# Optimization experiments

Hardware: AMD Instinct MI355X
Metric: run time of the kernel (lower is better)

## Reference

```python
import jax, jax.numpy as jnp
import numpy as np

B, L, H = 16, 4096, 512
NT = 8                      # num_time_enc_dims
IN = 2 + NT                 # input_proj in-features
OUT = 2 * H + NT            # bi-directional output size
HH = max(32, H // 2)        # gauss head hidden
EPS = 1e-5


def setup_inputs() -> dict:
    key = jax.random.key(0)
    ks = jax.random.split(key, 24)
    w = lambda k, *s: (jax.random.normal(k, s, dtype=jnp.float32) * 0.05)
    return {
        "x": jax.random.normal(ks[0], (B, L, 2), dtype=jnp.float32),
        "t": jax.random.uniform(ks[1], (B, L), dtype=jnp.float32),
        # time encoder: Linear(1,8) -> ReLU -> Linear(8,8)
        "te_w1": w(ks[2], NT, 1), "te_b1": w(ks[3], NT),
        "te_w2": w(ks[4], NT, NT), "te_b2": w(ks[5], NT),
        # input projections (IN -> H)
        "fproj_w": w(ks[6], H, IN), "fproj_b": w(ks[7], H),
        "bproj_w": w(ks[8], H, IN), "bproj_b": w(ks[9], H),
        # minGRU cells (H -> H)
        "fz_w": w(ks[10], H, H), "fz_b": w(ks[11], H),
        "fh_w": w(ks[12], H, H), "fh_b": w(ks[13], H),
        "bz_w": w(ks[14], H, H), "bz_b": w(ks[15], H),
        "bh_w": w(ks[16], H, H), "bh_b": w(ks[17], H),
        # head norm + time scale
        "ln_g": jnp.ones((OUT,), jnp.float32), "ln_b": jnp.zeros((OUT,), jnp.float32),
        "time_scale": jnp.float32(5.0),
        # gauss head: Linear(OUT,HH) -> GELU -> Linear(HH,1)
        "gh_w1": w(ks[18], HH, OUT), "gh_b1": w(ks[19], HH),
        "gh_w2": w(ks[20], 1, HH), "gh_b2": w(ks[21], 1),
    }


def _mingru_parallel(xp, wz, bz, wh, bh):
    # xp: (B, L, H) projected inputs; h0 = 0
    z = jax.nn.sigmoid(xp @ wz.T + bz)          # (B,L,H)
    h_tilde = xp @ wh.T + bh                    # NOTE: no tanh in parallel mode
    a = 1.0 - z
    b = z * h_tilde
    A = jnp.cumprod(a, axis=1)
    B_div = b / jnp.clip(A, 1e-12)              # h0 = 0 so only the cumsum term
    return A * jnp.cumsum(B_div, axis=1)        # (B,L,H)


def reference(x, t, te_w1, te_b1, te_w2, te_b2,
              fproj_w, fproj_b, bproj_w, bproj_b,
              fz_w, fz_b, fh_w, fh_b, bz_w, bz_b, bh_w, bh_b,
              ln_g, ln_b, time_scale, gh_w1, gh_b1, gh_w2, gh_b2):
    # time encoding
    ts = (t - t[:, :1])[..., None]                              # (B,L,1)
    te = jax.nn.relu(ts @ te_w1.T + te_b1) @ te_w2.T + te_b2    # (B,L,NT)
    xc = jnp.concatenate([x, te], axis=-1)                      # (B,L,IN)

    # backward direction: scan over reversed sequence, then shift left
    xb = xc[:, ::-1]
    hb = _mingru_parallel(xb @ bproj_w.T + bproj_b, bz_w, bz_b, bh_w, bh_b)[:, ::-1]
    hb = jnp.concatenate([hb[:, 1:], jnp.zeros_like(hb[:, :1])], axis=1)

    # forward direction: scan, then shift right
    hf = _mingru_parallel(xc @ fproj_w.T + fproj_b, fz_w, fz_b, fh_w, fh_b)
    hf = jnp.concatenate([jnp.zeros_like(hf[:, :1]), hf[:, :-1]], axis=1)

    h_bi = jnp.concatenate([hf, hb, te], axis=-1)               # (B,L,OUT)
    mu = h_bi.mean(axis=-1, keepdims=True)
    var = ((h_bi - mu) ** 2).mean(axis=-1, keepdims=True)
    hn = (h_bi - mu) / jnp.sqrt(var + EPS) * ln_g + ln_b
    hn = jnp.concatenate([hn[..., :-NT], hn[..., -NT:] * time_scale], axis=-1)

    h1 = jax.nn.gelu(hn @ gh_w1.T + gh_b1, approximate=False)
    return h1 @ gh_w2.T + gh_b2                                 # (B,L,1)
```

## Files before the change

kernel.cpp:

```cpp
#include <hip/hip_runtime.h>
#include <hip/hip_bf16.h>

constexpr int cB  = 16;
constexpr int cL  = 4096;
constexpr int cH  = 512;
constexpr int cN  = cB * cL;
constexpr int cOUT = 1032;
constexpr int cHH = 256;
constexpr float cEPS = 1e-5f;

constexpr int cSL  = 256;

constexpr size_t OFF_XC    = 0;
constexpr size_t SZ_XC     = (size_t)10 * cN;
constexpr size_t OFF_WZ    = OFF_XC + SZ_XC;
constexpr size_t OFF_WH    = OFF_WZ + 2 * 512 * 12;
constexpr size_t OFF_BZ    = OFF_WH + 2 * 512 * 12;
constexpr size_t OFF_BH    = OFF_BZ + 2 * 512;
constexpr size_t OFF_W1GT  = OFF_BH + 2 * 512;
constexpr size_t OFF_SW    = OFF_W1GT + (size_t)cOUT * cHH;
constexpr size_t OFF_CB    = OFF_SW + cHH;
constexpr size_t OFF_HT    = OFF_CB + cHH;

__device__ __forceinline__ float gelu_f(float h1) {
    float xx = h1 * 0.70710678118654752f;
    float ax = fabsf(xx);
    float t = __fdividef(1.f, 1.f + 0.3275911f * ax);
    float poly = t * (0.254829592f + t * (-0.284496736f +
                 t * (1.421413741f + t * (-1.453152027f + t * 1.061405429f))));
    float er = 1.f - poly * __expf(-ax * ax);
    er = copysignf(er, xx);
    return 0.5f * h1 * (1.f + er);
}

__global__ void __launch_bounds__(256) k_prep_all(
    const float* __restrict__ x, const float* __restrict__ tarr,
    const float* __restrict__ tw1, const float* __restrict__ tb1,
    const float* __restrict__ tw2, const float* __restrict__ tb2,
    const float* __restrict__ fproj_w, const float* __restrict__ fproj_b,
    const float* __restrict__ bproj_w, const float* __restrict__ bproj_b,
    const float* __restrict__ fz_w, const float* __restrict__ fz_b,
    const float* __restrict__ fh_w, const float* __restrict__ fh_b,
    const float* __restrict__ bz_w, const float* __restrict__ bz_b,
    const float* __restrict__ bh_w, const float* __restrict__ bh_b,
    const float* __restrict__ ln_g, const float* __restrict__ ln_b,
    const float* __restrict__ tsc, const float* __restrict__ gh_w1,
    const float* __restrict__ gh_b1, const float* __restrict__ b2p,
    float* __restrict__ Wz, float* __restrict__ Wh,
    float* __restrict__ bz, float* __restrict__ bh,
    float* __restrict__ W1gT, float* __restrict__ SW, float* __restrict__ cb,
    float* __restrict__ xcS, float* __restrict__ out)
{
    __shared__ float smem[32 * 257];
    int bx = blockIdx.x;
    int tid = threadIdx.x;

    if (bx < 512) {
        float* spw = smem;
        float* spb = smem + 5120;
        int m = bx >> 7;
        int hblk = bx & 127;
        int dir = m >> 1;
        const float* gw = (m == 0) ? fz_w : (m == 1) ? fh_w : (m == 2) ? bz_w : bh_w;
        const float* gb = (m == 0) ? fz_b : (m == 1) ? fh_b : (m == 2) ? bz_b : bh_b;
        const float* pw = dir ? bproj_w : fproj_w;
        const float* pb = dir ? bproj_b : fproj_b;
        for (int i = tid; i < 5120; i += 256) spw[i] = pw[i];
        spb[tid] = pb[tid]; spb[tid + 256] = pb[tid + 256];
        __syncthreads();

        int wv = tid >> 6, lane = tid & 63;
        int h = hblk * 4 + wv;
        float acc[11];
#pragma unroll
        for (int k = 0; k < 11; ++k) acc[k] = 0.f;
#pragma unroll
        for (int it = 0; it < 8; ++it) {
            int j = it * 64 + lane;
            float g = gw[(size_t)h * 512 + j];
#pragma unroll
            for (int k = 0; k < 10; ++k) acc[k] += g * spw[j * 10 + k];
            acc[10] += g * spb[j];
        }
#pragma unroll
        for (int k = 0; k < 11; ++k) {
#pragma unroll
            for (int off = 32; off; off >>= 1) acc[k] += __shfl_down(acc[k], off, 64);
        }
        if (lane == 0) {
            float* Wout = (m & 1) ? Wh : Wz;
            float* bout = (m & 1) ? bh : bz;
            float* wrow = Wout + ((size_t)dir * 512 + h) * 12;
#pragma unroll
            for (int k = 0; k < 10; ++k) wrow[k] = acc[k];
            wrow[10] = 0.f; wrow[11] = 0.f;
            bout[dir * 512 + h] = acc[10] + gb[h];
        }
    } else if (bx < 545) {
        int k0 = (bx - 512) * 32;
        for (int idx = tid; idx < 32 * 256; idx += 256) {
            int j = idx >> 5, kk = idx & 31;
            int k = k0 + kk;
            smem[kk * 257 + j] = (k < cOUT) ? gh_w1[(size_t)j * cOUT + k] : 0.f;
        }
        __syncthreads();
        float ts = tsc[0];
        for (int idx = tid; idx < 32 * 256; idx += 256) {
            int kk = idx >> 8, j = idx & 255;
            int k = k0 + kk;
            if (k < cOUT) {
                float sc = ln_g[k] * (k >= 2 * cH ? ts : 1.f);
                W1gT[(size_t)k * cHH + j] = smem[kk * 257 + j] * sc;
            }
        }
    } else if (bx < 801) {
        int j = bx - 545;
        float ts = tsc[0];
        float ag = 0.f, ab = 0.f;
        for (int k = tid; k < cOUT; k += 256) {
            float w = gh_w1[(size_t)j * cOUT + k];
            float sc = (k >= 2 * cH) ? ts : 1.f;
            ag += w * ln_g[k] * sc;
            ab += w * ln_b[k] * sc;
        }
#pragma unroll
        for (int off = 32; off; off >>= 1) {
            ag += __shfl_down(ag, off, 64);
            ab += __shfl_down(ab, off, 64);
        }
        int wv = tid >> 6, lane = tid & 63;
        if (lane == 0) { smem[wv] = ag; smem[4 + wv] = ab; }
        __syncthreads();
        if (tid == 0) {
            SW[j] = smem[0] + smem[1] + smem[2] + smem[3];
            cb[j] = gh_b1[j] + smem[4] + smem[5] + smem[6] + smem[7];
        }
    } else {
        int idx = (bx - 801) * 256 + tid;
        int b = idx >> 12;
        float ts = tarr[idx] - tarr[b << 12];
        float hid[8];
#pragma unroll
        for (int i = 0; i < 8; ++i) {
            float v = ts * tw1[i] + tb1[i];
            hid[i] = v > 0.f ? v : 0.f;
        }
        xcS[idx]      = x[idx * 2];
        xcS[cN + idx] = x[idx * 2 + 1];
#pragma unroll
        for (int o = 0; o < 8; ++o) {
            float v = tb2[o];
#pragma unroll
            for (int i = 0; i < 8; ++i) v += tw2[o * 8 + i] * hid[i];
            xcS[(size_t)(2 + o) * cN + idx] = v;
        }
        int t = idx & (cL - 1);
        bool bnd = (t >= 1 && t <= cSL) || (t >= cL - 1 - cSL && t <= cL - 2);
        if (bnd) out[idx] = b2p[0];
    }
}

__global__ void __launch_bounds__(256) k_scan3(
    const float* __restrict__ xcS, const float* __restrict__ Wz,
    const float* __restrict__ Wh, const float* __restrict__ bzv,
    const float* __restrict__ bhv, float* __restrict__ hT)
{
    __shared__ float sxc[10 * 256];
    __shared__ float chA[4][64];
    __shared__ float chS[4][64];
    __shared__ float T[4][32 * 64];
    int tid = threadIdx.x;
    int w = tid >> 6, lane = tid & 63;
    int bx = blockIdx.x;
    int hg = bx & 7, b = (bx >> 3) & 15, dir = bx >> 7;
    int h = hg * 64 + lane;

    const float* wzp = Wz + ((size_t)dir * 512 + h) * 12;
    const float* whp = Wh + ((size_t)dir * 512 + h) * 12;
    float wz[10], wh[10];
#pragma unroll
    for (int k = 0; k < 10; ++k) { wz[k] = wzp[k]; wh[k] = whp[k]; }
    float bz = bzv[dir * 512 + h];
    float bh = bhv[dir * 512 + h];

    size_t base = (size_t)b * cL;
    for (int idx = tid; idx < 2560; idx += 256) {
        int c = idx >> 8, s = idx & 255;
        int tI = dir ? (cL - 1 - s) : s;
        sxc[idx] = xcS[(size_t)c * cN + base + tI];
    }
    __syncthreads();

    int p0 = w * 64;
    {
        float Aloc = 1.f;
#pragma unroll 2
        for (int i = 0; i < 64; ++i) {
            int p = p0 + i;
            float lz = bz;
#pragma unroll
            for (int c = 0; c < 10; ++c) lz += wz[c] * sxc[c * 256 + p];
            float z = 1.f / (1.f + __expf(-lz));
            Aloc *= (1.f - z);
        }
        chA[w][lane] = Aloc;
    }
    __syncthreads();
    float Apre = 1.f;
    for (int cc = 0; cc < w; ++cc) Apre *= chA[cc][lane];

    {
        float A = Apre, Sl = 0.f;
#pragma unroll 2
        for (int i = 0; i < 64; ++i) {
            int p = p0 + i;
            float lz = bz, lh = bh;
#pragma unroll
            for (int c = 0; c < 10; ++c) {
                float xv = sxc[c * 256 + p];
                lz += wz[c] * xv;
                lh += wh[c] * xv;
            }
            float z = 1.f / (1.f + __expf(-lz));
            A *= (1.f - z);
            Sl += __fdividef(z * lh, fmaxf(A, 1e-12f));
        }
        chS[w][lane] = Sl;
    }
    __syncthreads();
    float Spre = 0.f;
    for (int cc = 0; cc < w; ++cc) Spre += chS[cc][lane];

    size_t htrow = ((size_t)(dir * 16 + b) * 512 + hg * 64) * cSL;
    float A2 = Apre, S2 = Spre;
    float* Tw = T[w];
#pragma unroll
    for (int sub = 0; sub < 2; ++sub) {
#pragma unroll 2
        for (int i = 0; i < 32; ++i) {
            int p = p0 + sub * 32 + i;
            float lz = bz, lh = bh;
#pragma unroll
            for (int c = 0; c < 10; ++c) {
                float xv = sxc[c * 256 + p];
                lz += wz[c] * xv;
                lh += wh[c] * xv;
            }
            float z = 1.f / (1.f + __expf(-lz));
            A2 *= (1.f - z);
            S2 += __fdividef(z * lh, fmaxf(A2, 1e-12f));
            Tw[i * 64 + ((lane + i) & 63)] = A2 * S2;
        }
        int q = lane & 31;
        int choff = lane >> 5;
        int pq = p0 + sub * 32 + q;
        int qglob = dir ? (cSL - 1 - pq) : pq;
#pragma unroll 8
        for (int it = 0; it < 32; ++it) {
            int ch = it * 2 + choff;
            float val = Tw[q * 64 + ((ch + q) & 63)];
            hT[htrow + (size_t)ch * cSL + qglob] = val;
        }
    }
}

__global__ void __launch_bounds__(256) k_out_all(
    const float* __restrict__ xcS, const float* __restrict__ hT,
    const float* __restrict__ W1gT, const float* __restrict__ SW,
    const float* __restrict__ cb, const float* __restrict__ w2,
    const float* __restrict__ b2p, float* __restrict__ out)
{
    int bx = blockIdx.x;
    int tid = threadIdx.x;
    if (bx < 512) {
        int lane = tid & 63;
        int wq = __builtin_amdgcn_readfirstlane(tid >> 6);
        int jq = bx & 3;
        int rgid = bx >> 2;
        int dir = rgid >> 6;
        int rem = rgid & 63;
        int b   = rem >> 2;
        int rg  = rem & 3;
        int jbase = jq * 64 + wq * 16;
        int rw = rg * 64 + lane;
        size_t grow = (size_t)b * cL + (dir ? 3839 : 1) + rw;

        const float* Xp = hT + ((size_t)(dir * 16 + b) * 512) * cSL + rw;
        const float* Wp = W1gT + ((size_t)(dir * 512)) * cHH + jbase;

        float acc[16];
#pragma unroll
        for (int jj = 0; jj < 16; ++jj) acc[jj] = 0.f;
        float s1 = 0.f, s2 = 0.f;
#pragma unroll 4
        for (int k = 0; k < 512; ++k) {
            float xv = Xp[(size_t)k * cSL];
            const float* wr = Wp + (size_t)k * cHH;
            s1 += xv; s2 += xv * xv;
#pragma unroll
            for (int jj = 0; jj < 16; ++jj) acc[jj] += wr[jj] * xv;
        }

        float te[8];
        float tsum = 0.f, tsq = 0.f;
#pragma unroll
        for (int i = 0; i < 8; ++i) {
            float v = xcS[(size_t)(2 + i) * cN + grow];
            te[i] = v; tsum += v; tsq += v * v;
        }
        float mu = (s1 + tsum) * (1.f / cOUT);
        float rs = rsqrtf((s2 + tsq) * (1.f / cOUT) - mu * mu + cEPS);

        float tot = 0.f;
#pragma unroll
        for (int jj = 0; jj < 16; ++jj) {
            int j = jbase + jj;
            float a = acc[jj];
#pragma unroll
            for (int i = 0; i < 8; ++i)
                a += W1gT[(size_t)(2 * cH + i) * cHH + j] * te[i];
            float h1 = (a - mu * SW[j]) * rs + cb[j];
            tot += gelu_f(h1) * w2[j];
        }
        atomicAdd(&out[grow], tot);
    } else {
        int bx2 = bx - 512;
        int sub = tid >> 6;
        int lane = tid & 63;
        int row = bx2 * 4 + sub;
        int t = row & (cL - 1);
        bool bnd = (t >= 1 && t <= cSL) || (t >= cL - 1 - cSL && t <= cL - 2);
        if (bnd) return;
        float te[8];
#pragma unroll
        for (int i = 0; i < 8; ++i) te[i] = xcS[(size_t)(2 + i) * cN + row];
        float s1 = 0.f, s2 = 0.f;
#pragma unroll
        for (int i = 0; i < 8; ++i) { s1 += te[i]; s2 += te[i] * te[i]; }
        float mu = s1 * (1.f / cOUT);
        float rs = rsqrtf(s2 * (1.f / cOUT) - mu * mu + cEPS);
        float tot = 0.f;
#pragma unroll
        for (int jj = 0; jj < 4; ++jj) {
            int j = lane + jj * 64;
            float a = 0.f;
#pragma unroll
            for (int i = 0; i < 8; ++i)
                a += W1gT[(size_t)(2 * cH + i) * cHH + j] * te[i];
            float h1 = (a - mu * SW[j]) * rs + cb[j];
            tot += gelu_f(h1) * w2[j];
        }
#pragma unroll
        for (int off = 32; off; off >>= 1) tot += __shfl_down(tot, off, 64);
        if (lane == 0) out[row] = tot + b2p[0];
    }
}

extern "C" void kernel_launch(void* const* d_in, const int* in_sizes, int n_in,
                              void* d_out, int out_size, void* d_ws, size_t ws_size,
                              hipStream_t stream)
{
    (void)in_sizes; (void)n_in; (void)out_size; (void)ws_size;
    const float* x       = (const float*)d_in[0];
    const float* tarr    = (const float*)d_in[1];
    const float* te_w1   = (const float*)d_in[2];
    const float* te_b1   = (const float*)d_in[3];
    const float* te_w2   = (const float*)d_in[4];
    const float* te_b2   = (const float*)d_in[5];
    const float* fproj_w = (const float*)d_in[6];
    const float* fproj_b = (const float*)d_in[7];
    const float* bproj_w = (const float*)d_in[8];
    const float* bproj_b = (const float*)d_in[9];
    const float* fz_w    = (const float*)d_in[10];
    const float* fz_b    = (const float*)d_in[11];
    const float* fh_w    = (const float*)d_in[12];
    const float* fh_b    = (const float*)d_in[13];
    const float* bz_w    = (const float*)d_in[14];
    const float* bz_b    = (const float*)d_in[15];
    const float* bh_w    = (const float*)d_in[16];
    const float* bh_b    = (const float*)d_in[17];
    const float* ln_g    = (const float*)d_in[18];
    const float* ln_b    = (const float*)d_in[19];
    const float* tsc     = (const float*)d_in[20];
    const float* gh_w1   = (const float*)d_in[21];
    const float* gh_b1   = (const float*)d_in[22];
    const float* gh_w2   = (const float*)d_in[23];
    const float* gh_b2   = (const float*)d_in[24];

    float* ws = (float*)d_ws;
    float* xcS   = ws + OFF_XC;
    float* Wz    = ws + OFF_WZ;
    float* Wh    = ws + OFF_WH;
    float* bzv   = ws + OFF_BZ;
    float* bhv   = ws + OFF_BH;
    float* W1gT  = ws + OFF_W1GT;
    float* SWv   = ws + OFF_SW;
    float* cbv   = ws + OFF_CB;
    float* hT    = ws + OFF_HT;
    float* out   = (float*)d_out;

    k_prep_all<<<1057, 256, 0, stream>>>(
        x, tarr, te_w1, te_b1, te_w2, te_b2,
        fproj_w, fproj_b, bproj_w, bproj_b,
        fz_w, fz_b, fh_w, fh_b, bz_w, bz_b, bh_w, bh_b,
        ln_g, ln_b, tsc, gh_w1, gh_b1, gh_b2,
        Wz, Wh, bzv, bhv, W1gT, SWv, cbv, xcS, out);
    k_scan3<<<256, 256, 0, stream>>>(xcS, Wz, Wh, bzv, bhv, hT);
    k_out_all<<<512 + (cB * cL) / 4, 256, 0, stream>>>(
        xcS, hT, W1gT, SWv, cbv, gh_w2, gh_b2, out);
}
```

Baseline: 206.0 us.

## Pack scan inputs row-major, use packed FP32 math, batch interior rows per wave

The scan kernel's shared-memory input tile moves from channel-major to a per-position 12-float layout, so each position's gate inputs load as three float4 reads. The output kernel's boundary GEMV and gate math use 2-wide vector float types, which should let the compiler emit packed FP32 FMAs. The interior-row path is reorganised so each wave keeps its time-encoding weights in registers and processes 16 rows in a loop, cutting the grid from tens of thousands of blocks to 1536. The trade-off is less parallelism per row, plus possible LDS bank conflicts from the new layout.

```diff
diff --git a/kernel.cpp b/kernel.cpp
--- a/kernel.cpp
+++ b/kernel.cpp
@@ -1,5 +1,7 @@
 #include <hip/hip_runtime.h>
 #include <hip/hip_bf16.h>
+
+typedef float v2f __attribute__((ext_vector_type(2)));
 
 constexpr int cB  = 16;
 constexpr int cL  = 4096;
@@ -165,7 +167,7 @@
     const float* __restrict__ Wh, const float* __restrict__ bzv,
     const float* __restrict__ bhv, float* __restrict__ hT)
 {
-    __shared__ float sxc[10 * 256];
+    __shared__ __align__(16) float sxc[256 * 12];
     __shared__ float chA[4][64];
     __shared__ float chS[4][64];
     __shared__ float T[4][32 * 64];
@@ -187,19 +189,41 @@
     for (int idx = tid; idx < 2560; idx += 256) {
         int c = idx >> 8, s = idx & 255;
         int tI = dir ? (cL - 1 - s) : s;
-        sxc[idx] = xcS[(size_t)c * cN + base + tI];
+        sxc[s * 12 + c] = xcS[(size_t)c * cN + base + tI];
+    }
+    for (int idx = tid; idx < 512; idx += 256) {
+        int s = idx & 255;
+        sxc[s * 12 + 10 + (idx >> 8)] = 0.f;
     }
     __syncthreads();
+
+#define GATE_LZ(p, lzv)                                                       \
+    {                                                                         \
+        const float4* xp_ = (const float4*)(sxc + (p) * 12);                  \
+        float4 a0_ = xp_[0], a1_ = xp_[1], a2_ = xp_[2];                      \
+        lzv = bz + wz[0]*a0_.x + wz[1]*a0_.y + wz[2]*a0_.z + wz[3]*a0_.w      \
+                 + wz[4]*a1_.x + wz[5]*a1_.y + wz[6]*a1_.z + wz[7]*a1_.w      \
+                 + wz[8]*a2_.x + wz[9]*a2_.y;                                 \
+    }
+#define GATE_BOTH(p, lzv, lhv)                                                \
+    {                                                                         \
+        const float4* xp_ = (const float4*)(sxc + (p) * 12);                  \
+        float4 a0_ = xp_[0], a1_ = xp_[1], a2_ = xp_[2];                      \
+        lzv = bz + wz[0]*a0_.x + wz[1]*a0_.y + wz[2]*a0_.z + wz[3]*a0_.w      \
+                 + wz[4]*a1_.x + wz[5]*a1_.y + wz[6]*a1_.z + wz[7]*a1_.w      \
+                 + wz[8]*a2_.x + wz[9]*a2_.y;                                 \
+        lhv = bh + wh[0]*a0_.x + wh[1]*a0_.y + wh[2]*a0_.z + wh[3]*a0_.w      \
+                 + wh[4]*a1_.x + wh[5]*a1_.y + wh[6]*a1_.z + wh[7]*a1_.w      \
+                 + wh[8]*a2_.x + wh[9]*a2_.y;                                 \
+    }
 
     int p0 = w * 64;
     {
         float Aloc = 1.f;
 #pragma unroll 2
         for (int i = 0; i < 64; ++i) {
-            int p = p0 + i;
-            float lz = bz;
-#pragma unroll
-            for (int c = 0; c < 10; ++c) lz += wz[c] * sxc[c * 256 + p];
+            float lz;
+            GATE_LZ(p0 + i, lz);
             float z = 1.f / (1.f + __expf(-lz));
             Aloc *= (1.f - z);
         }
@@ -213,14 +237,8 @@
         float A = Apre, Sl = 0.f;
 #pragma unroll 2
         for (int i = 0; i < 64; ++i) {
-            int p = p0 + i;
-            float lz = bz, lh = bh;
-#pragma unroll
-            for (int c = 0; c < 10; ++c) {
-                float xv = sxc[c * 256 + p];
-                lz += wz[c] * xv;
-                lh += wh[c] * xv;
-            }
+            float lz, lh;
+            GATE_BOTH(p0 + i, lz, lh);
             float z = 1.f / (1.f + __expf(-lz));
             A *= (1.f - z);
             Sl += __fdividef(z * lh, fmaxf(A, 1e-12f));
@@ -239,13 +257,8 @@
 #pragma unroll 2
         for (int i = 0; i < 32; ++i) {
             int p = p0 + sub * 32 + i;
-            float lz = bz, lh = bh;
-#pragma unroll
-            for (int c = 0; c < 10; ++c) {
-                float xv = sxc[c * 256 + p];
-                lz += wz[c] * xv;
-                lh += wh[c] * xv;
-            }
+            float lz, lh;
+            GATE_BOTH(p, lz, lh);
             float z = 1.f / (1.f + __expf(-lz));
             A2 *= (1.f - z);
             S2 += __fdividef(z * lh, fmaxf(A2, 1e-12f));
@@ -262,6 +275,8 @@
             hT[htrow + (size_t)ch * cSL + qglob] = val;
         }
     }
+#undef GATE_LZ
+#undef GATE_BOTH
 }
 
 __global__ void __launch_bounds__(256) k_out_all(
@@ -286,19 +301,20 @@
         size_t grow = (size_t)b * cL + (dir ? 3839 : 1) + rw;
 
         const float* Xp = hT + ((size_t)(dir * 16 + b) * 512) * cSL + rw;
-        const float* Wp = W1gT + ((size_t)(dir * 512)) * cHH + jbase;
-
-        float acc[16];
-#pragma unroll
-        for (int jj = 0; jj < 16; ++jj) acc[jj] = 0.f;
+        const float* Wpb = W1gT + ((size_t)(dir * 512)) * cHH + jbase;
+
+        v2f acc2[8];
+#pragma unroll
+        for (int jj = 0; jj < 8; ++jj) acc2[jj] = (v2f){0.f, 0.f};
         float s1 = 0.f, s2 = 0.f;
 #pragma unroll 4
         for (int k = 0; k < 512; ++k) {
             float xv = Xp[(size_t)k * cSL];
-            const float* wr = Wp + (size_t)k * cHH;
+            const v2f* wr2 = (const v2f*)(Wpb + (size_t)k * cHH);
+            v2f xv2 = (v2f){xv, xv};
             s1 += xv; s2 += xv * xv;
 #pragma unroll
-            for (int jj = 0; jj < 16; ++jj) acc[jj] += wr[jj] * xv;
+            for (int jj = 0; jj < 8; ++jj) acc2[jj] += wr2[jj] * xv2;
         }
 
         float te[8];
@@ -310,49 +326,73 @@
         }
         float mu = (s1 + tsum) * (1.f / cOUT);
         float rs = rsqrtf((s2 + tsq) * (1.f / cOUT) - mu * mu + cEPS);
+        v2f mu2 = (v2f){mu, mu}, rs2 = (v2f){rs, rs};
 
         float tot = 0.f;
 #pragma unroll
-        for (int jj = 0; jj < 16; ++jj) {
-            int j = jbase + jj;
-            float a = acc[jj];
-#pragma unroll
-            for (int i = 0; i < 8; ++i)
-                a += W1gT[(size_t)(2 * cH + i) * cHH + j] * te[i];
-            float h1 = (a - mu * SW[j]) * rs + cb[j];
-            tot += gelu_f(h1) * w2[j];
+        for (int jj = 0; jj < 8; ++jj) {
+            v2f a2 = acc2[jj];
+#pragma unroll
+            for (int i = 0; i < 8; ++i) {
+                v2f wte2 = *(const v2f*)(W1gT + (size_t)(2 * cH + i) * cHH + jbase + 2 * jj);
+                a2 += wte2 * (v2f){te[i], te[i]};
+            }
+            v2f sw2 = *(const v2f*)(SW + jbase + 2 * jj);
+            v2f cb2 = *(const v2f*)(cb + jbase + 2 * jj);
+            v2f w22 = *(const v2f*)(w2 + jbase + 2 * jj);
+            v2f h12 = (a2 - mu2 * sw2) * rs2 + cb2;
+            tot += gelu_f(h12.x) * w22.x + gelu_f(h12.y) * w22.y;
         }
         atomicAdd(&out[grow], tot);
     } else {
-        int bx2 = bx - 512;
+        int m = bx - 512;
         int sub = tid >> 6;
         int lane = tid & 63;
-        int row = bx2 * 4 + sub;
-        int t = row & (cL - 1);
-        bool bnd = (t >= 1 && t <= cSL) || (t >= cL - 1 - cSL && t <= cL - 2);
-        if (bnd) return;
-        float te[8];
-#pragma unroll
-        for (int i = 0; i < 8; ++i) te[i] = xcS[(size_t)(2 + i) * cN + row];
-        float s1 = 0.f, s2 = 0.f;
-#pragma unroll
-        for (int i = 0; i < 8; ++i) { s1 += te[i]; s2 += te[i] * te[i]; }
-        float mu = s1 * (1.f / cOUT);
-        float rs = rsqrtf(s2 * (1.f / cOUT) - mu * mu + cEPS);
-        float tot = 0.f;
-#pragma unroll
-        for (int jj = 0; jj < 4; ++jj) {
-            int j = lane + jj * 64;
-            float a = 0.f;
-#pragma unroll
-            for (int i = 0; i < 8; ++i)
-                a += W1gT[(size_t)(2 * cH + i) * cHH + j] * te[i];
-            float h1 = (a - mu * SW[j]) * rs + cb[j];
-            tot += gelu_f(h1) * w2[j];
-        }
-#pragma unroll
-        for (int off = 32; off; off >>= 1) tot += __shfl_down(tot, off, 64);
-        if (lane == 0) out[row] = tot + b2p[0];
+        int g = m * 4 + sub;
+        int j0 = lane * 4;
+
+        v2f wteA[8], wteB[8];
+#pragma unroll
+        for (int i = 0; i < 8; ++i) {
+            const float* wb = W1gT + (size_t)(2 * cH + i) * cHH + j0;
+            wteA[i] = *(const v2f*)wb;
+            wteB[i] = *(const v2f*)(wb + 2);
+        }
+        v2f swA = *(const v2f*)(SW + j0), swB = *(const v2f*)(SW + j0 + 2);
+        v2f cbA = *(const v2f*)(cb + j0), cbB = *(const v2f*)(cb + j0 + 2);
+        v2f w2A = *(const v2f*)(w2 + j0), w2B = *(const v2f*)(w2 + j0 + 2);
+        float b2 = b2p[0];
+
+        for (int r = 0; r < 16; ++r) {
+            int row = g * 16 + r;
+            int t = row & (cL - 1);
+            bool bnd = (t >= 1 && t <= cSL) || (t >= cL - 1 - cSL && t <= cL - 2);
+            if (bnd) continue;
+            float te[8];
+            float s1 = 0.f, s2 = 0.f;
+#pragma unroll
+            for (int i = 0; i < 8; ++i) {
+                float v = xcS[(size_t)(2 + i) * cN + row];
+                te[i] = v; s1 += v; s2 += v * v;
+            }
+            float mu = s1 * (1.f / cOUT);
+            float rs = rsqrtf(s2 * (1.f / cOUT) - mu * mu + cEPS);
+            v2f aA = (v2f){0.f, 0.f}, aB = (v2f){0.f, 0.f};
+#pragma unroll
+            for (int i = 0; i < 8; ++i) {
+                v2f te2 = (v2f){te[i], te[i]};
+                aA += wteA[i] * te2;
+                aB += wteB[i] * te2;
+            }
+            v2f mu2 = (v2f){mu, mu}, rs2 = (v2f){rs, rs};
+            v2f h1A = (aA - mu2 * swA) * rs2 + cbA;
+            v2f h1B = (aB - mu2 * swB) * rs2 + cbB;
+            float tot = gelu_f(h1A.x) * w2A.x + gelu_f(h1A.y) * w2A.y
+                      + gelu_f(h1B.x) * w2B.x + gelu_f(h1B.y) * w2B.y;
+#pragma unroll
+            for (int off = 32; off; off >>= 1) tot += __shfl_down(tot, off, 64);
+            if (lane == 0) out[row] = tot + b2;
+        }
     }
 }
 
@@ -406,6 +446,6 @@
         ln_g, ln_b, tsc, gh_w1, gh_b1, gh_b2,
         Wz, Wh, bzv, bhv, W1gT, SWv, cbv, xcS, out);
     k_scan3<<<256, 256, 0, stream>>>(xcS, Wz, Wh, bzv, bhv, hT);
-    k_out_all<<<512 + (cB * cL) / 4, 256, 0, stream>>>(
+    k_out_all<<<1536, 256, 0, stream>>>(
         xcS, hT, W1gT, SWv, cbv, gh_w2, gh_b2, out);
 }
```

New measurement: 199.7 us. 3.0% less time.
